# Kernel optimization log

Hardware: AMD Instinct MI355X
Metric: run time of the kernel (lower is better)

Reference implementation:

```python
import jax, jax.numpy as jnp
import numpy as np

N_NODES = 100000
N_EDGES = 1600000
IN_DIM = 64
HID = 128
OUT_DIM = 2
N_GRAPHS = 64


def setup_inputs() -> dict:
    key = jax.random.key(0)
    ks = jax.random.split(key, 9)
    x = jax.random.normal(ks[0], (N_NODES, IN_DIM), dtype=jnp.float32)
    edge_index = jax.random.randint(ks[1], (2, N_EDGES), 0, N_NODES, dtype=jnp.int64)
    batch = jnp.sort(jax.random.randint(ks[2], (N_NODES,), 0, N_GRAPHS, dtype=jnp.int64))
    # GCNConv weights (Glorot-ish scale) and biases
    W1 = jax.random.normal(ks[3], (IN_DIM, HID), dtype=jnp.float32) / np.sqrt(IN_DIM)
    b1 = jnp.zeros((HID,), dtype=jnp.float32)
    W2 = jax.random.normal(ks[4], (HID, HID), dtype=jnp.float32) / np.sqrt(HID)
    b2 = jnp.zeros((HID,), dtype=jnp.float32)
    Wfc = jax.random.normal(ks[5], (HID, OUT_DIM), dtype=jnp.float32) / np.sqrt(HID)
    bfc = jnp.zeros((OUT_DIM,), dtype=jnp.float32)
    return {"x": x, "W1": W1, "b1": b1, "W2": W2, "b2": b2,
            "Wfc": Wfc, "bfc": bfc, "edge_index": edge_index, "batch": batch}


def _gcn_conv(x, W, b, src, dst, num_nodes):
    # PyG GCNConv: linear transform, add self loops, symmetric deg norm, scatter-add.
    h = x @ W  # [N, F]
    loop = jnp.arange(num_nodes, dtype=src.dtype)
    s = jnp.concatenate([src, loop])  # source (message origin)
    d = jnp.concatenate([dst, loop])  # target (aggregation)
    deg = jax.ops.segment_sum(jnp.ones_like(d, dtype=h.dtype), d, num_segments=num_nodes)
    dinv = jnp.where(deg > 0, jax.lax.rsqrt(deg), 0.0)
    norm = dinv[s] * dinv[d]  # [E+N]
    msg = h[s] * norm[:, None]
    out = jax.ops.segment_sum(msg, d, num_segments=num_nodes)
    return out + b


def reference(x, W1, b1, W2, b2, Wfc, bfc, edge_index, batch):
    src, dst = edge_index[0], edge_index[1]
    n = x.shape[0]
    h = jax.nn.relu(_gcn_conv(x, W1, b1, src, dst, n))
    # dropout is a no-op in eval mode
    h = jax.nn.relu(_gcn_conv(h, W2, b2, src, dst, n))
    # global mean pool over graphs
    sums = jax.ops.segment_sum(h, batch, num_segments=N_GRAPHS)
    cnts = jax.ops.segment_sum(jnp.ones((n,), dtype=h.dtype), batch, num_segments=N_GRAPHS)
    pooled = sums / jnp.maximum(cnts, 1.0)[:, None]  # [G, HID]
    logits = pooled @ Wfc + bfc
    return jax.nn.log_softmax(logits, axis=1)
```

## Files before the change

### kernel.cpp

```cpp
#include <hip/hip_runtime.h>
#include <math.h>

#define N_NODES 100000
#define N_EDGES 1600000
#define IN_DIM 64
#define HID 128
#define OUT_DIM 2
#define N_GRAPHS 64

#define NBUK ((N_NODES + 255) / 256)
#define BCAP 4608
#define E4 (N_EDGES / 4)
#define NBLK_P1 ((E4 + 1023) / 1024)

#define PCHUNK 256
#define MAXCH 8

typedef unsigned int uint32;
typedef __attribute__((ext_vector_type(8))) short bf16x8;
typedef __attribute__((ext_vector_type(4))) float f32x4;

static __device__ __forceinline__ ushort f2bf(float f) {
    uint32 u = __float_as_uint(f);
    uint32 r = (u + 0x7fff + ((u >> 16) & 1)) >> 16;
    return (ushort)r;
}
static __device__ __forceinline__ float bf2f(uint32 u) {
    return __uint_as_float(u << 16);
}
static __device__ __forceinline__ float bflo(uint32 u) { return bf2f(u & 0xffffu); }
static __device__ __forceinline__ float bfhi(uint32 u) { return bf2f(u >> 16); }

__global__ __launch_bounds__(1024) void k_pass1(const int4* __restrict__ src4,
                                                const int4* __restrict__ dst4,
                                                int* __restrict__ gcur,
                                                int* __restrict__ bpak) {
    __shared__ int hist[NBUK];
    __shared__ int base[NBUK];
    int tid = threadIdx.x;
    if (tid < NBUK) hist[tid] = 0;
    __syncthreads();
    int i4 = blockIdx.x * 1024 + tid;
    bool act = i4 < E4;
    int4 d = {0, 0, 0, 0}, s = {0, 0, 0, 0};
    if (act) {
        d = dst4[i4];
        s = src4[i4];
        atomicAdd(&hist[d.x >> 8], 1);
        atomicAdd(&hist[d.y >> 8], 1);
        atomicAdd(&hist[d.z >> 8], 1);
        atomicAdd(&hist[d.w >> 8], 1);
    }
    __syncthreads();
    if (tid < NBUK) {
        int c = hist[tid];
        base[tid] = tid * BCAP + (c ? atomicAdd(&gcur[tid], c) : 0);
        hist[tid] = 0;
    }
    __syncthreads();
    if (act) {
        int b0 = d.x >> 8, r0 = atomicAdd(&hist[b0], 1);
        int b1 = d.y >> 8, r1 = atomicAdd(&hist[b1], 1);
        int b2 = d.z >> 8, r2 = atomicAdd(&hist[b2], 1);
        int b3 = d.w >> 8, r3 = atomicAdd(&hist[b3], 1);
        bpak[base[b0] + r0] = ((d.x & 255) << 24) | s.x;
        bpak[base[b1] + r1] = ((d.y & 255) << 24) | s.y;
        bpak[base[b2] + r2] = ((d.z & 255) << 24) | s.z;
        bpak[base[b3] + r3] = ((d.w & 255) << 24) | s.w;
    }
}

__global__ __launch_bounds__(1024) void k_pass2(const int* __restrict__ gcur,
                                                const int* __restrict__ bpak,
                                                const float* __restrict__ x,
                                                const int* __restrict__ batch,
                                                int* __restrict__ row_start,
                                                float* __restrict__ dinv,
                                                int* __restrict__ csr,
                                                ushort* __restrict__ xs,
                                                int* __restrict__ gstart) {
    __shared__ int cnt[256];
    __shared__ int sc[256];
    __shared__ int lst[256];
    __shared__ float sdinv[256];
    __shared__ int sg[1024];
    __shared__ int sgb;
    int b = blockIdx.x;
    int tid = threadIdx.x;
    int node0 = b * 256;
    int nloc = N_NODES - node0;
    if (nloc > 256) nloc = 256;
    int bbase = b * BCAP;
    int Eb = gcur[b];

    sg[tid] = (tid < NBUK) ? gcur[tid] : 0;
    if (tid < 256) cnt[tid] = 0;
    __syncthreads();
    for (int off = 1; off < 512; off <<= 1) {
        int u = (tid >= off) ? sg[tid - off] : 0;
        __syncthreads();
        sg[tid] += u;
        __syncthreads();
    }
    if (tid == 0) sgb = (b == 0) ? 0 : sg[b - 1];
    __syncthreads();
    int gb = sgb;

    for (int i = tid; i < Eb; i += 1024) atomicAdd(&cnt[(uint32)bpak[bbase + i] >> 24], 1);
    __syncthreads();
    int v = 0;
    if (tid < 256) {
        v = cnt[tid];
        sc[tid] = v;
    }
    __syncthreads();
    for (int off = 1; off < 256; off <<= 1) {
        int u = 0;
        if (tid < 256 && tid >= off) u = sc[tid - off];
        __syncthreads();
        if (tid < 256) sc[tid] += u;
        __syncthreads();
    }
    if (tid < 256) {
        int excl = sc[tid] - v;
        lst[tid] = excl;
        if (tid < nloc) {
            int n = node0 + tid;
            float dv = rsqrtf((float)(v + 1));
            row_start[n] = gb + excl;
            dinv[n] = dv;
            sdinv[tid] = dv;
            if (n == 0) {
                for (int g = 0; g <= batch[0]; ++g) gstart[g] = 0;
            } else {
                int a = batch[n - 1], bb = batch[n];
                for (int g = a + 1; g <= bb; ++g) gstart[g] = n;
            }
            if (n == N_NODES - 1) {
                for (int g = batch[n] + 1; g <= N_GRAPHS; ++g) gstart[g] = N_NODES;
                row_start[N_NODES] = N_EDGES;
            }
        }
        cnt[tid] = 0;
    }
    __syncthreads();
    for (int i = tid; i < Eb; i += 1024) {
        int p = bpak[bbase + i];
        int dl = (uint32)p >> 24;
        int r = atomicAdd(&cnt[dl], 1);
        csr[gb + lst[dl] + r] = p & 0xFFFFFF;
    }
    int f0 = node0 * 16;
    int f1 = (node0 + nloc) * 16;
    for (int idx = f0 + tid; idx < f1; idx += 1024) {
        float dv = sdinv[(idx >> 4) - node0];
        float4 vv = ((const float4*)x)[idx];
        ushort4 o;
        o.x = f2bf(vv.x * dv);
        o.y = f2bf(vv.y * dv);
        o.z = f2bf(vv.z * dv);
        o.w = f2bf(vv.w * dv);
        ((ushort4*)xs)[idx] = o;
    }
}

__global__ __launch_bounds__(256) void k_agg1(const int* __restrict__ row_start,
                                              const int* __restrict__ csr,
                                              const uint32* __restrict__ xs,
                                              const float* __restrict__ dinv,
                                              uint32* __restrict__ outb) {
    int d = blockIdx.x * 8 + (threadIdx.x >> 5);
    int l = threadIdx.x & 31;
    float dd = dinv[d];
    uint32 u = xs[(long long)d * 32 + l];
    float a0 = bflo(u), a1 = bfhi(u);
    int e = row_start[d];
    int eend = row_start[d + 1];
    for (; e + 7 < eend; e += 8) {
        int s0 = csr[e], s1 = csr[e + 1], s2 = csr[e + 2], s3 = csr[e + 3];
        int s4 = csr[e + 4], s5 = csr[e + 5], s6 = csr[e + 6], s7 = csr[e + 7];
        uint32 w0 = xs[(long long)s0 * 32 + l];
        uint32 w1 = xs[(long long)s1 * 32 + l];
        uint32 w2 = xs[(long long)s2 * 32 + l];
        uint32 w3 = xs[(long long)s3 * 32 + l];
        uint32 w4 = xs[(long long)s4 * 32 + l];
        uint32 w5 = xs[(long long)s5 * 32 + l];
        uint32 w6 = xs[(long long)s6 * 32 + l];
        uint32 w7 = xs[(long long)s7 * 32 + l];
        a0 += ((bflo(w0) + bflo(w1)) + (bflo(w2) + bflo(w3))) +
              ((bflo(w4) + bflo(w5)) + (bflo(w6) + bflo(w7)));
        a1 += ((bfhi(w0) + bfhi(w1)) + (bfhi(w2) + bfhi(w3))) +
              ((bfhi(w4) + bfhi(w5)) + (bfhi(w6) + bfhi(w7)));
    }
    for (; e + 3 < eend; e += 4) {
        int s0 = csr[e], s1 = csr[e + 1], s2 = csr[e + 2], s3 = csr[e + 3];
        uint32 w0 = xs[(long long)s0 * 32 + l];
        uint32 w1 = xs[(long long)s1 * 32 + l];
        uint32 w2 = xs[(long long)s2 * 32 + l];
        uint32 w3 = xs[(long long)s3 * 32 + l];
        a0 += (bflo(w0) + bflo(w1)) + (bflo(w2) + bflo(w3));
        a1 += (bfhi(w0) + bfhi(w1)) + (bfhi(w2) + bfhi(w3));
    }
    for (; e < eend; ++e) {
        uint32 w = xs[(long long)csr[e] * 32 + l];
        a0 += bflo(w);
        a1 += bfhi(w);
    }
    outb[(long long)d * 32 + l] = (uint32)f2bf(a0 * dd) | ((uint32)f2bf(a1 * dd) << 16);
}

__global__ __launch_bounds__(256) void k_agg2(const int* __restrict__ row_start,
                                              const int* __restrict__ csr,
                                              const uint2* __restrict__ hs,
                                              const float* __restrict__ dinv,
                                              uint2* __restrict__ outb) {
    int d = blockIdx.x * 8 + (threadIdx.x >> 5);
    int l = threadIdx.x & 31;
    float dd = dinv[d];
    uint2 u = hs[(long long)d * 32 + l];
    float a0 = bflo(u.x), a1 = bfhi(u.x), a2 = bflo(u.y), a3 = bfhi(u.y);
    int e = row_start[d];
    int eend = row_start[d + 1];
    for (; e + 7 < eend; e += 8) {
        int s0 = csr[e], s1 = csr[e + 1], s2 = csr[e + 2], s3 = csr[e + 3];
        int s4 = csr[e + 4], s5 = csr[e + 5], s6 = csr[e + 6], s7 = csr[e + 7];
        uint2 w0 = hs[(long long)s0 * 32 + l];
        uint2 w1 = hs[(long long)s1 * 32 + l];
        uint2 w2 = hs[(long long)s2 * 32 + l];
        uint2 w3 = hs[(long long)s3 * 32 + l];
        uint2 w4 = hs[(long long)s4 * 32 + l];
        uint2 w5 = hs[(long long)s5 * 32 + l];
        uint2 w6 = hs[(long long)s6 * 32 + l];
        uint2 w7 = hs[(long long)s7 * 32 + l];
        a0 += ((bflo(w0.x) + bflo(w1.x)) + (bflo(w2.x) + bflo(w3.x))) +
              ((bflo(w4.x) + bflo(w5.x)) + (bflo(w6.x) + bflo(w7.x)));
        a1 += ((bfhi(w0.x) + bfhi(w1.x)) + (bfhi(w2.x) + bfhi(w3.x))) +
              ((bfhi(w4.x) + bfhi(w5.x)) + (bfhi(w6.x) + bfhi(w7.x)));
        a2 += ((bflo(w0.y) + bflo(w1.y)) + (bflo(w2.y) + bflo(w3.y))) +
              ((bflo(w4.y) + bflo(w5.y)) + (bflo(w6.y) + bflo(w7.y)));
        a3 += ((bfhi(w0.y) + bfhi(w1.y)) + (bfhi(w2.y) + bfhi(w3.y))) +
              ((bfhi(w4.y) + bfhi(w5.y)) + (bfhi(w6.y) + bfhi(w7.y)));
    }
    for (; e + 3 < eend; e += 4) {
        int s0 = csr[e], s1 = csr[e + 1], s2 = csr[e + 2], s3 = csr[e + 3];
        uint2 w0 = hs[(long long)s0 * 32 + l];
        uint2 w1 = hs[(long long)s1 * 32 + l];
        uint2 w2 = hs[(long long)s2 * 32 + l];
        uint2 w3 = hs[(long long)s3 * 32 + l];
        a0 += (bflo(w0.x) + bflo(w1.x)) + (bflo(w2.x) + bflo(w3.x));
        a1 += (bfhi(w0.x) + bfhi(w1.x)) + (bfhi(w2.x) + bfhi(w3.x));
        a2 += (bflo(w0.y) + bflo(w1.y)) + (bflo(w2.y) + bflo(w3.y));
        a3 += (bfhi(w0.y) + bfhi(w1.y)) + (bfhi(w2.y) + bfhi(w3.y));
    }
    for (; e < eend; ++e) {
        uint2 w = hs[(long long)csr[e] * 32 + l];
        a0 += bflo(w.x);
        a1 += bfhi(w.x);
        a2 += bflo(w.y);
        a3 += bfhi(w.y);
    }
    uint2 o;
    o.x = (uint32)f2bf(a0 * dd) | ((uint32)f2bf(a1 * dd) << 16);
    o.y = (uint32)f2bf(a2 * dd) | ((uint32)f2bf(a3 * dd) << 16);
    outb[(long long)d * 32 + l] = o;
}

template <int K, int OUTM>
__global__ __launch_bounds__(256) void k_gemm_mfma(const ushort* __restrict__ A,
                                                   const float* __restrict__ W,
                                                   const float* __restrict__ bias,
                                                   const float* __restrict__ dinv,
                                                   ushort* __restrict__ outb) {
    constexpr int KSTEPS = K / 32;
    constexpr int LDSK = K + 8;
    __shared__ ushort WT[128 * LDSK];
    int tid = threadIdx.x;
    for (int idx = tid; idx < K * 128; idx += 256) {
        int k = idx >> 7, c = idx & 127;
        WT[c * LDSK + k] = f2bf(W[idx]);
    }
    __syncthreads();

    int w = tid >> 6, l = tid & 63;
    int row0 = blockIdx.x * 64 + w * 16;
    int arow = row0 + (l & 15);
    if (arow > N_NODES - 1) arow = N_NODES - 1;
    int koff = (l >> 4) * 8;

    bf16x8 af[KSTEPS];
#pragma unroll
    for (int ks = 0; ks < KSTEPS; ++ks)
        af[ks] = *(const bf16x8*)(A + (long long)arow * K + ks * 32 + koff);

    f32x4 acc[8];
#pragma unroll
    for (int t = 0; t < 8; ++t) acc[t] = (f32x4){0.f, 0.f, 0.f, 0.f};

#pragma unroll
    for (int ks = 0; ks < KSTEPS; ++ks) {
#pragma unroll
        for (int t = 0; t < 8; ++t) {
            int c = t * 16 + (l & 15);
            bf16x8 bf = *(const bf16x8*)&WT[c * LDSK + ks * 32 + koff];
            acc[t] = __builtin_amdgcn_mfma_f32_16x16x32_bf16(af[ks], bf, acc[t], 0, 0, 0);
        }
    }

    int rbase = row0 + ((l >> 4) << 2);
#pragma unroll
    for (int t = 0; t < 8; ++t) {
        int col = t * 16 + (l & 15);
        float bb = bias[col];
#pragma unroll
        for (int i = 0; i < 4; ++i) {
            int row = rbase + i;
            if (row < N_NODES) {
                float v = acc[t][i] + bb;
                v = v > 0.f ? v : 0.f;
                if (OUTM == 1) v *= dinv[row];
                outb[(long long)row * HID + col] = f2bf(v);
            }
        }
    }
}

__global__ __launch_bounds__(256) void k_pool(const uint32* __restrict__ h2,
                                              const int* __restrict__ gstart,
                                              float* __restrict__ pooled) {
    int g = blockIdx.x >> 3;
    int c = blockIdx.x & (MAXCH - 1);
    int r0 = gstart[g] + c * PCHUNK;
    int r1 = gstart[g + 1];
    if (r0 >= r1) return;
    int rend = r0 + PCHUNK;
    if (rend > r1) rend = r1;
    int j = threadIdx.x & 63;
    int q = threadIdx.x >> 6;
    float a0 = 0.f, a1 = 0.f, b0 = 0.f, b1 = 0.f;
    int r = r0 + q;
    for (; r + 4 < rend; r += 8) {
        uint32 u = h2[(long long)r * 64 + j];
        uint32 v = h2[(long long)(r + 4) * 64 + j];
        a0 += bflo(u);
        a1 += bfhi(u);
        b0 += bflo(v);
        b1 += bfhi(v);
    }
    for (; r < rend; r += 4) {
        uint32 u = h2[(long long)r * 64 + j];
        a0 += bflo(u);
        a1 += bfhi(u);
    }
    __shared__ float red[256][2];
    red[threadIdx.x][0] = a0 + b0;
    red[threadIdx.x][1] = a1 + b1;
    __syncthreads();
    if (q == 0) {
        float s0 = (red[j][0] + red[j + 64][0]) + (red[j + 128][0] + red[j + 192][0]);
        float s1 = (red[j][1] + red[j + 64][1]) + (red[j + 128][1] + red[j + 192][1]);
        atomicAdd(&pooled[g * HID + 2 * j], s0);
        atomicAdd(&pooled[g * HID + 2 * j + 1], s1);
    }
}

__global__ __launch_bounds__(256) void k_head(const float* __restrict__ pooled,
                                              const int* __restrict__ gstart,
                                              const float* __restrict__ Wfc,
                                              const float* __restrict__ bfc,
                                              float* __restrict__ out) {
    int t = threadIdx.x;
    int g = t >> 2, sub = t & 3;
    float inv = 1.0f / fmaxf((float)(gstart[g + 1] - gstart[g]), 1.0f);
    float l0 = 0.f, l1 = 0.f;
    for (int j = sub * 32; j < sub * 32 + 32; ++j) {
        float p = pooled[g * HID + j] * inv;
        l0 += p * Wfc[j * OUT_DIM + 0];
        l1 += p * Wfc[j * OUT_DIM + 1];
    }
    l0 += __shfl_xor(l0, 1);
    l1 += __shfl_xor(l1, 1);
    l0 += __shfl_xor(l0, 2);
    l1 += __shfl_xor(l1, 2);
    if (sub == 0) {
        l0 += bfc[0];
        l1 += bfc[1];
        float m = fmaxf(l0, l1);
        float lse = m + logf(expf(l0 - m) + expf(l1 - m));
        out[g * OUT_DIM + 0] = l0 - lse;
        out[g * OUT_DIM + 1] = l1 - lse;
    }
}

extern "C" void kernel_launch(void* const* d_in, const int* in_sizes, int n_in,
                              void* d_out, int out_size, void* d_ws, size_t ws_size,
                              hipStream_t stream) {
    const float* x   = (const float*)d_in[0];
    const float* W1  = (const float*)d_in[1];
    const float* b1  = (const float*)d_in[2];
    const float* W2  = (const float*)d_in[3];
    const float* b2  = (const float*)d_in[4];
    const float* Wfc = (const float*)d_in[5];
    const float* bfc = (const float*)d_in[6];
    const int* ei    = (const int*)d_in[7];
    const int* batch = (const int*)d_in[8];
    const int* src = ei;
    const int* dst = ei + N_EDGES;
    float* out = (float*)d_out;

    float* bufA = (float*)d_ws;
    float* bufB = bufA + (long long)N_NODES * HID;
    int* bpak = (int*)bufA;
    ushort* agg1o = (ushort*)bufA;
    ushort* agg2o = (ushort*)bufA;
    ushort* xs = (ushort*)bufB;
    ushort* hs = (ushort*)bufB;
    ushort* h2 = (ushort*)bufB;
    int* row_start = (int*)(bufB + (long long)N_NODES * HID);
    float* dinv = (float*)(row_start + N_NODES + 1);
    int* gcur = (int*)(dinv + N_NODES);
    int* gstart = gcur + NBUK;
    int* csr = gstart + (N_GRAPHS + 1);
    float* pooled = (float*)(csr + N_EDGES);

    hipMemsetAsync(gcur, 0, NBUK * sizeof(int), stream);
    hipMemsetAsync(pooled, 0, N_GRAPHS * HID * sizeof(float), stream);
    k_pass1<<<NBLK_P1, 1024, 0, stream>>>((const int4*)src, (const int4*)dst, gcur, bpak);
    k_pass2<<<NBUK, 1024, 0, stream>>>(gcur, bpak, x, batch, row_start, dinv, csr, xs, gstart);

    const int NGBLK = (N_NODES + 63) / 64;

    k_agg1<<<N_NODES / 8, 256, 0, stream>>>(row_start, csr, (const uint32*)xs, dinv,
                                            (uint32*)agg1o);
    k_gemm_mfma<IN_DIM, 1><<<NGBLK, 256, 0, stream>>>(agg1o, W1, b1, dinv, hs);

    k_agg2<<<N_NODES / 8, 256, 0, stream>>>(row_start, csr, (const uint2*)hs, dinv,
                                            (uint2*)agg2o);
    k_gemm_mfma<HID, 2><<<NGBLK, 256, 0, stream>>>(agg2o, W2, b2, dinv, h2);

    k_pool<<<N_GRAPHS * MAXCH, 256, 0, stream>>>((const uint32*)h2, gstart, pooled);
    k_head<<<1, 256, 0, stream>>>(pooled, gstart, Wfc, bfc, out);
}
```

Baseline: 212.3 us.

## Fuse global mean-pool into second GEMM epilogue, dropping h2 store and pool kernel

The second GCN layer's GEMM epilogue now applies bias and ReLU and then accumulates per-graph column sums straight into LDS, using the sorted batch vector to split each 64-row block into at most two graphs. Block partials are then atomically added to the global pooled buffer. This removes the write and re-read of the full 100k×128 bf16 h2 tensor and one kernel launch. In exchange it adds LDS atomics, about 1563×256 global float atomics, and relies on batch being sorted so that a 64-row block spans no more than two graphs.

```diff
diff --git a/kernel.cpp b/kernel.cpp
--- a/kernel.cpp
+++ b/kernel.cpp
@@ -12,9 +12,6 @@
 #define BCAP 4608
 #define E4 (N_EDGES / 4)
 #define NBLK_P1 ((E4 + 1023) / 1024)
-
-#define PCHUNK 256
-#define MAXCH 8
 
 typedef unsigned int uint32;
 typedef __attribute__((ext_vector_type(8))) short bf16x8;
@@ -270,14 +267,22 @@
                                                    const float* __restrict__ W,
                                                    const float* __restrict__ bias,
                                                    const float* __restrict__ dinv,
-                                                   ushort* __restrict__ outb) {
+                                                   ushort* __restrict__ outb,
+                                                   const int* __restrict__ batch,
+                                                   float* __restrict__ pooled) {
     constexpr int KSTEPS = K / 32;
     constexpr int LDSK = K + 8;
     __shared__ ushort WT[128 * LDSK];
+    __shared__ float pcA[128];
+    __shared__ float pcB[128];
     int tid = threadIdx.x;
     for (int idx = tid; idx < K * 128; idx += 256) {
         int k = idx >> 7, c = idx & 127;
         WT[c * LDSK + k] = f2bf(W[idx]);
+    }
+    if (OUTM == 3 && tid < 128) {
+        pcA[tid] = 0.f;
+        pcB[tid] = 0.f;
     }
     __syncthreads();
 
@@ -307,59 +312,56 @@
     }
 
     int rbase = row0 + ((l >> 4) << 2);
-#pragma unroll
-    for (int t = 0; t < 8; ++t) {
-        int col = t * 16 + (l & 15);
-        float bb = bias[col];
+    if (OUTM == 1) {
+#pragma unroll
+        for (int t = 0; t < 8; ++t) {
+            int col = t * 16 + (l & 15);
+            float bb = bias[col];
+#pragma unroll
+            for (int i = 0; i < 4; ++i) {
+                int row = rbase + i;
+                if (row < N_NODES) {
+                    float v = acc[t][i] + bb;
+                    v = v > 0.f ? v : 0.f;
+                    outb[(long long)row * HID + col] = f2bf(v * dinv[row]);
+                }
+            }
+        }
+    } else {
+        int blk0 = blockIdx.x * 64;
+        int lastrow = blk0 + 63;
+        if (lastrow > N_NODES - 1) lastrow = N_NODES - 1;
+        int g0 = batch[blk0];
+        int g1 = batch[lastrow];
+        bool twoseg = (g1 != g0);
+        int bg[4];
 #pragma unroll
         for (int i = 0; i < 4; ++i) {
             int row = rbase + i;
-            if (row < N_NODES) {
-                float v = acc[t][i] + bb;
-                v = v > 0.f ? v : 0.f;
-                if (OUTM == 1) v *= dinv[row];
-                outb[(long long)row * HID + col] = f2bf(v);
+            bg[i] = (row < N_NODES) ? batch[row] : -1;
+        }
+#pragma unroll
+        for (int t = 0; t < 8; ++t) {
+            int col = t * 16 + (l & 15);
+            float bb = bias[col];
+            float sA = 0.f, sB = 0.f;
+#pragma unroll
+            for (int i = 0; i < 4; ++i) {
+                if (bg[i] >= 0) {
+                    float v = acc[t][i] + bb;
+                    v = v > 0.f ? v : 0.f;
+                    if (bg[i] == g0) sA += v;
+                    else sB += v;
+                }
             }
-        }
-    }
-}
-
-__global__ __launch_bounds__(256) void k_pool(const uint32* __restrict__ h2,
-                                              const int* __restrict__ gstart,
-                                              float* __restrict__ pooled) {
-    int g = blockIdx.x >> 3;
-    int c = blockIdx.x & (MAXCH - 1);
-    int r0 = gstart[g] + c * PCHUNK;
-    int r1 = gstart[g + 1];
-    if (r0 >= r1) return;
-    int rend = r0 + PCHUNK;
-    if (rend > r1) rend = r1;
-    int j = threadIdx.x & 63;
-    int q = threadIdx.x >> 6;
-    float a0 = 0.f, a1 = 0.f, b0 = 0.f, b1 = 0.f;
-    int r = r0 + q;
-    for (; r + 4 < rend; r += 8) {
-        uint32 u = h2[(long long)r * 64 + j];
-        uint32 v = h2[(long long)(r + 4) * 64 + j];
-        a0 += bflo(u);
-        a1 += bfhi(u);
-        b0 += bflo(v);
-        b1 += bfhi(v);
-    }
-    for (; r < rend; r += 4) {
-        uint32 u = h2[(long long)r * 64 + j];
-        a0 += bflo(u);
-        a1 += bfhi(u);
-    }
-    __shared__ float red[256][2];
-    red[threadIdx.x][0] = a0 + b0;
-    red[threadIdx.x][1] = a1 + b1;
-    __syncthreads();
-    if (q == 0) {
-        float s0 = (red[j][0] + red[j + 64][0]) + (red[j + 128][0] + red[j + 192][0]);
-        float s1 = (red[j][1] + red[j + 64][1]) + (red[j + 128][1] + red[j + 192][1]);
-        atomicAdd(&pooled[g * HID + 2 * j], s0);
-        atomicAdd(&pooled[g * HID + 2 * j + 1], s1);
+            atomicAdd(&pcA[col], sA);
+            if (twoseg) atomicAdd(&pcB[col], sB);
+        }
+        __syncthreads();
+        if (tid < 128) {
+            atomicAdd(&pooled[g0 * HID + tid], pcA[tid]);
+            if (twoseg) atomicAdd(&pooled[g1 * HID + tid], pcB[tid]);
+        }
     }
 }
 
@@ -414,7 +416,6 @@
     ushort* agg2o = (ushort*)bufA;
     ushort* xs = (ushort*)bufB;
     ushort* hs = (ushort*)bufB;
-    ushort* h2 = (ushort*)bufB;
     int* row_start = (int*)(bufB + (long long)N_NODES * HID);
     float* dinv = (float*)(row_start + N_NODES + 1);
     int* gcur = (int*)(dinv + N_NODES);
@@ -431,12 +432,13 @@
 
     k_agg1<<<N_NODES / 8, 256, 0, stream>>>(row_start, csr, (const uint32*)xs, dinv,
                                             (uint32*)agg1o);
-    k_gemm_mfma<IN_DIM, 1><<<NGBLK, 256, 0, stream>>>(agg1o, W1, b1, dinv, hs);
+    k_gemm_mfma<IN_DIM, 1><<<NGBLK, 256, 0, stream>>>(agg1o, W1, b1, dinv, hs, nullptr,
+                                                      nullptr);
 
     k_agg2<<<N_NODES / 8, 256, 0, stream>>>(row_start, csr, (const uint2*)hs, dinv,
                                             (uint2*)agg2o);
-    k_gemm_mfma<HID, 2><<<NGBLK, 256, 0, stream>>>(agg2o, W2, b2, dinv, h2);
-
-    k_pool<<<N_GRAPHS * MAXCH, 256, 0, stream>>>((const uint32*)h2, gstart, pooled);
+    k_gemm_mfma<HID, 3><<<NGBLK, 256, 0, stream>>>(agg2o, W2, b2, dinv, nullptr, batch,
+                                                   pooled);
+
     k_head<<<1, 256, 0, stream>>>(pooled, gstart, Wfc, bfc, out);
 }
```

New measurement: 208.4 us. Within noise of the previous version (-1.8%).
